# Kernel optimization log

Measured on AMD Instinct MI355X. Metric: run time of the kernel, lower is better.

## Reference

```python
import jax, jax.numpy as jnp
import numpy as np

S, B, E, H = 192, 2, 512, 2
D = E // H      # head_dim = 256 == E/2; required so attn_fc(3*D) matches concat of three E/2 chunks
BH = B * H

def _lin(x, W, b):
    return x @ W.T + b

def setup_inputs():
    key = jax.random.key(0)
    ks = jax.random.split(key, 16)
    p = lambda k, *s: jax.random.normal(k, s, jnp.float32) * 0.02
    return {
        "query":       jax.random.normal(ks[0], (S, B, E), jnp.float32),
        "entity":      jax.random.normal(ks[1], (S, B, E), jnp.float32),
        "ex_entity":   jax.random.normal(ks[2], (S, B, B, E), jnp.float32),
        "ex_relation": jax.random.normal(ks[3], (S, B, B, E), jnp.float32),
        "Wq": p(ks[4], D, E), "bq": jnp.zeros((D,), jnp.float32),
        "Wk": p(ks[5], D, E), "bk": jnp.zeros((D,), jnp.float32),
        "Wv": p(ks[6], D, E), "bv": jnp.zeros((D,), jnp.float32),
        "We": p(ks[7], D, E), "be": jnp.zeros((D,), jnp.float32),
        "Wxe": p(ks[8], D, E), "bxe": jnp.zeros((D,), jnp.float32),
        "Wxr": p(ks[9], D, E), "bxr": jnp.zeros((D,), jnp.float32),
        "Wa": p(ks[10], 1, 3 * D), "ba": jnp.zeros((1,), jnp.float32),
        "Wo": p(ks[11], E, E), "bo": jnp.zeros((E,), jnp.float32),
    }

def reference(query, entity, ex_entity, ex_relation,
              Wq, bq, Wk, bk, Wv, bv, We, be, Wxe, bxe, Wxr, bxr, Wa, ba, Wo, bo):
    e = _lin(entity, We, be)            # [S,B,D]
    q = _lin(query, Wq, bq)             # [S,B,D]
    exr = _lin(ex_entity, Wxe, bxe)     # exent_proj(ex_entity) -> [S,B,B,D]
    exe = _lin(ex_relation, Wxr, bxr)   # exrel_proj(ex_relation) -> [S,B,B,D]
    e_b = jnp.broadcast_to(e[:, :, None, :], exe.shape)
    exz = jnp.concatenate([exe, e_b, exr], axis=-1)                              # [S,B,B,3D]
    exw = jax.nn.softmax(jax.nn.leaky_relu((exz @ Wa.T + ba)[..., 0]), axis=-1)  # [S,B,B]
    we = jnp.einsum('sbk,skd->sbd', exw, e)  # torch.bmm; dead when en_tgt==tgt (faithful fwd compute)
    del we
    qe = jnp.concatenate([q, e], axis=-1)    # [S,B,E]  (else-branch: e.size(0)==q.size(0))
    k = _lin(query, Wk, bk)
    v = _lin(query, Wv, bv)
    ke = jnp.concatenate([k, e], axis=-1)
    ve = jnp.concatenate([v, e], axis=-1)
    shp = lambda x: jnp.swapaxes(x.reshape(S, BH, D), 0, 1)  # torch _shape -> [BH,S,D]
    qe_s, ke_s, ve_s = shp(qe), shp(ke), shp(ve)
    # edge[i,j,b,:] = entity[i,b] - entity[j,b]; torch then does a flat .view(BH,S,S,D)
    edge = (entity[:, None] - entity[None, :]).reshape(BH, S, S, D)
    # qe: transpose(0,1).repeat(S,1,1,1).transpose(0,1).reshape -> broadcast over src then flat reshape
    qe_r = jnp.broadcast_to(jnp.swapaxes(qe_s, 0, 1)[:, None], (S, S, BH, D)).reshape(BH, S, S, D)
    # ke: repeat(S,1,1,1).reshape (flat)
    ke_r = jnp.broadcast_to(ke_s[None], (S, BH, S, D)).reshape(BH, S, S, D)
    z = jnp.concatenate([qe_r, ke_r, edge], axis=-1)                             # [BH,S,S,3D]
    aw = jax.nn.softmax(jax.nn.leaky_relu((z @ Wa.T + ba)[..., 0]), axis=-1)     # [BH,S,S]
    out = jnp.einsum('bts,bsd->btd', aw, ve_s)                                   # [BH,S,D]
    out = jnp.swapaxes(out, 0, 1).reshape(S, B, E)
    return _lin(out, Wo, bo)
```

## Files before the change

### kernel.cpp

```cpp
#include <hip/hip_runtime.h>
#include <math.h>


#define SS 192
#define VO  0
#define EO  98304
#define TO  196608
#define OO  198912
#define WTV 395520
#define WTE 526592
#define WTO 657664

__device__ __forceinline__ float wave_reduce_add(float p) {
    #pragma unroll
    for (int off = 32; off >= 1; off >>= 1) p += __shfl_xor(p, off, 64);
    return p;
}

__global__ __launch_bounds__(1024) void k_prep(
    const float* __restrict__ query, const float* __restrict__ entity,
    const float* __restrict__ Wq, const float* __restrict__ bq,
    const float* __restrict__ Wk, const float* __restrict__ bk,
    const float* __restrict__ Wv, const float* __restrict__ We,
    const float* __restrict__ be, const float* __restrict__ Wa,
    const float* __restrict__ Wo, float* __restrict__ ws)
{
    __shared__ __align__(16) float red[16 * 512];
    __shared__ __align__(16) float uo[516];
    int blk = blockIdx.x;
    int tid = threadIdx.x;

    if (blk < 128) {
        int o = blk * 1024 + tid;
        const float4* src; float4* dst; int idx; int D;
        if (o < 32768)      { src = (const float4*)Wv; dst = (float4*)(ws + WTV); idx = o;         D = 256; }
        else if (o < 65536) { src = (const float4*)We; dst = (float4*)(ws + WTE); idx = o - 32768; D = 256; }
        else                { src = (const float4*)Wo; dst = (float4*)(ws + WTO); idx = o - 65536; D = 512; }
        int d  = idx >> 7;
        int k4 = idx & 127;
        dst[k4 * D + d] = src[idx];
        return;
    }

    int wv   = __builtin_amdgcn_readfirstlane(tid >> 6);
    int lane = tid & 63;

    if (blk < 136) {
        int tab = blk - 128;
        int p   = (tab < 4) ? tab : tab - 4;
        int b   = p >> 1, h = p & 1;
        const float* wa   = Wa + ((tab < 4) ? 0 : 256);
        const float* W    = h ? We : ((tab < 4) ? Wq : Wk);
        const float* bias = h ? be : ((tab < 4) ? bq : bk);
        const float* x    = h ? entity : query;

        float u8[8];
        #pragma unroll
        for (int i = 0; i < 8; i++) u8[i] = 0.f;
        #pragma unroll 4
        for (int dd = 0; dd < 16; dd++) {
            int d = wv * 16 + dd;
            float wad = wa[d];
            const float4* Wr = (const float4*)(W + (size_t)d * 512);
            float4 w0 = Wr[lane * 2], w1 = Wr[lane * 2 + 1];
            u8[0] += wad * w0.x; u8[1] += wad * w0.y; u8[2] += wad * w0.z; u8[3] += wad * w0.w;
            u8[4] += wad * w1.x; u8[5] += wad * w1.y; u8[6] += wad * w1.z; u8[7] += wad * w1.w;
        }
        #pragma unroll
        for (int i = 0; i < 8; i++) red[wv * 512 + lane * 8 + i] = u8[i];
        __syncthreads();
        if (tid < 512) {
            float s = 0.f;
            #pragma unroll
            for (int w = 0; w < 16; w++) s += red[w * 512 + tid];
            uo[tid] = s;
        }
        __syncthreads();
        if (tid < 256) red[tid] = wa[tid] * bias[tid];
        __syncthreads();
        for (int o = 128; o >= 1; o >>= 1) {
            if (tid < o) red[tid] += red[tid + o];
            __syncthreads();
        }
        float off = red[0];

        const float4* u4 = (const float4*)uo;
        float4 ua = u4[lane * 2], ub = u4[lane * 2 + 1];
        for (int rr = 0; rr < 12; rr++) {
            int r = wv * 12 + rr;
            const float4* xr = (const float4*)(x + (size_t)(r * 2 + b) * 512);
            float4 a0 = xr[lane * 2], a1 = xr[lane * 2 + 1];
            float pp = a0.x*ua.x + a0.y*ua.y + a0.z*ua.z + a0.w*ua.w
                     + a1.x*ub.x + a1.y*ub.y + a1.z*ub.z + a1.w*ub.w;
            pp = wave_reduce_add(pp);
            if (lane == 0) ws[TO + tab * SS + r] = pp + off;
        }
        return;
    }

    {
        int m = blk - 136;
        float4 wa4 = ((const float4*)(Wa + 512))[lane];
        for (int rr = 0; rr < 12; rr++) {
            int i = wv * 12 + rr;
            const float4* er = (const float4*)(entity
                + (size_t)(i * 2 + (m >> 1)) * 512 + (m & 1) * 256);
            float4 e4 = er[lane];
            float pp = e4.x*wa4.x + e4.y*wa4.y + e4.z*wa4.z + e4.w*wa4.w;
            pp = wave_reduce_add(pp);
            if (lane == 0) ws[TO + (8 + m) * SS + i] = pp;
        }
    }
}

__global__ __launch_bounds__(1024) void k_proj(
    const float* __restrict__ query, const float* __restrict__ entity,
    const float* __restrict__ bv, const float* __restrict__ be,
    float* __restrict__ ws)
{
    __shared__ float lds[4096];
    int blk = blockIdx.x;
    int m  = blk / 96;
    int r0 = (blk % 96) * 4;
    int tid = threadIdx.x;
    int chunk = __builtin_amdgcn_readfirstlane(tid >> 8);
    int d  = tid & 255;
    const float*  A    = m ? entity : query;
    const float*  bias = m ? be : bv;
    const float4* WT   = (const float4*)(ws + (m ? WTE : WTV));
    float*        dst  = ws + (m ? EO : VO);
    const float4* A4   = (const float4*)A;

    float acc[4];
    #pragma unroll
    for (int r = 0; r < 4; r++) acc[r] = 0.f;

    int k4b = chunk * 32;
    #pragma unroll 8
    for (int i = 0; i < 32; i++) {
        int k4 = k4b + i;
        float4 w = WT[k4 * 256 + d];
        #pragma unroll
        for (int r = 0; r < 4; r++) {
            float4 a = A4[(r0 + r) * 128 + k4];
            acc[r] += a.x * w.x + a.y * w.y + a.z * w.z + a.w * w.w;
        }
    }
    #pragma unroll
    for (int r = 0; r < 4; r++) lds[(chunk * 4 + r) * 256 + d] = acc[r];
    __syncthreads();
    {
        int idx = tid;
        int rr  = idx >> 8, dd = idx & 255;
        float v = lds[idx] + lds[1024 + idx] + lds[2048 + idx] + lds[3072 + idx];
        dst[(size_t)(r0 + rr) * 256 + dd] = v + bias[dd];
    }
}

__global__ __launch_bounds__(1024) void k_attn(
    const float* __restrict__ ba_p, float* __restrict__ ws)
{
    __shared__ __align__(16) float lds[4096];
    __shared__ __align__(16) float sp4[768];
    int blk = blockIdx.x;
    int bh = blk & 3;
    int tg = blk >> 2;
    int b = bh >> 1, h = bh & 1;
    const float* T = ws + TO;
    float ba = ba_p[0];
    int tid  = threadIdx.x;
    int wv   = __builtin_amdgcn_readfirstlane(tid >> 6);
    int lane = tid & 63;

    if (wv < 4) {
        int ti = wv;
        int i_idx = bh * 48 + tg;
        float sc[3]; float mx = -1e30f;
        #pragma unroll
        for (int i = 0; i < 3; i++) {
            int s_ = lane + 64 * i;
            int m  = s_ & 3;
            int j  = ti * 48 + (s_ >> 2);
            float xv = T[m * SS + i_idx] + T[(4 + ti) * SS + s_]
                     + T[(8 + m) * SS + i_idx] - T[(8 + m) * SS + j] + ba;
            xv = (xv >= 0.f) ? xv : 0.01f * xv;
            sc[i] = xv; mx = fmaxf(mx, xv);
        }
        #pragma unroll
        for (int o = 32; o >= 1; o >>= 1) mx = fmaxf(mx, __shfl_xor(mx, o, 64));
        float sum = 0.f;
        #pragma unroll
        for (int i = 0; i < 3; i++) { sc[i] = __expf(sc[i] - mx); sum += sc[i]; }
        sum = wave_reduce_add(sum);
        float inv = 1.f / sum;
        #pragma unroll
        for (int i = 0; i < 3; i++) sp4[ti * SS + lane + 64 * i] = sc[i] * inv;
    }
    __syncthreads();

    int sq = __builtin_amdgcn_readfirstlane(tid >> 8);
    int dd = tid & 255;
    const float* src = ws + (h ? EO : VO) + b * 256 + dd;
    float a[4] = {0.f, 0.f, 0.f, 0.f};
    #pragma unroll 8
    for (int s2 = 0; s2 < 48; s2++) {
        int s = sq * 48 + s2;
        float xv = src[(size_t)s * 512];
        #pragma unroll
        for (int ti = 0; ti < 4; ti++) a[ti] += sp4[ti * SS + s] * xv;
    }
    #pragma unroll
    for (int ti = 0; ti < 4; ti++) lds[sq * 1024 + ti * 256 + dd] = a[ti];
    __syncthreads();
    {
        int ti = tid >> 8, d2 = tid & 255;
        int idx = ti * 256 + d2;
        float v = lds[idx] + lds[1024 + idx] + lds[2048 + idx] + lds[3072 + idx];
        int t = tg * 4 + ti;
        ws[OO + (size_t)(2 * t + b) * 512 + h * 256 + d2] = v;
    }
}

__global__ __launch_bounds__(1024) void k_out(
    const float* __restrict__ bo, const float* __restrict__ ws,
    float* __restrict__ out)
{
    __shared__ float lds[4096];
    int blk = blockIdx.x;
    int rg = blk >> 1;
    int cg = blk & 1;
    int r0 = rg * 4;
    int tid = threadIdx.x;
    int chunk = __builtin_amdgcn_readfirstlane(tid >> 8);
    int col = cg * 256 + (tid & 255);
    const float4* A4 = (const float4*)(ws + OO);
    const float4* WT = (const float4*)(ws + WTO);

    float acc[4];
    #pragma unroll
    for (int r = 0; r < 4; r++) acc[r] = 0.f;

    int k4b = chunk * 32;
    #pragma unroll 8
    for (int i = 0; i < 32; i++) {
        int k4 = k4b + i;
        float4 w = WT[k4 * 512 + col];
        #pragma unroll
        for (int r = 0; r < 4; r++) {
            float4 a = A4[(r0 + r) * 128 + k4];
            acc[r] += a.x * w.x + a.y * w.y + a.z * w.z + a.w * w.w;
        }
    }
    int dl = tid & 255;
    #pragma unroll
    for (int r = 0; r < 4; r++) lds[(chunk * 4 + r) * 256 + dl] = acc[r];
    __syncthreads();
    {
        int idx = tid;
        int rr = idx >> 8, d2 = idx & 255;
        float v = lds[idx] + lds[1024 + idx] + lds[2048 + idx] + lds[3072 + idx];
        out[(size_t)(r0 + rr) * 512 + cg * 256 + d2] = v + bo[cg * 256 + d2];
    }
}

extern "C" void kernel_launch(void* const* d_in, const int* in_sizes, int n_in,
                              void* d_out, int out_size, void* d_ws, size_t ws_size,
                              hipStream_t stream) {
    const float* query  = (const float*)d_in[0];
    const float* entity = (const float*)d_in[1];
    const float* Wq = (const float*)d_in[4];  const float* bq = (const float*)d_in[5];
    const float* Wk = (const float*)d_in[6];  const float* bk = (const float*)d_in[7];
    const float* Wv = (const float*)d_in[8];  const float* bv = (const float*)d_in[9];
    const float* We = (const float*)d_in[10]; const float* be = (const float*)d_in[11];
    const float* Wa = (const float*)d_in[16]; const float* ba = (const float*)d_in[17];
    const float* Wo = (const float*)d_in[18]; const float* bo = (const float*)d_in[19];
    float* ws  = (float*)d_ws;
    float* out = (float*)d_out;

    hipLaunchKernelGGL(k_prep, dim3(140), dim3(1024), 0, stream,
                       query, entity, Wq, bq, Wk, bk, Wv, We, be, Wa, Wo, ws);
    hipLaunchKernelGGL(k_proj, dim3(192), dim3(1024), 0, stream,
                       query, entity, bv, be, ws);
    hipLaunchKernelGGL(k_attn, dim3(192), dim3(1024), 0, stream, ba, ws);
    hipLaunchKernelGGL(k_out,  dim3(192), dim3(1024), 0, stream, bo, ws, out);
}
```

Before: 48.90 us.

## Fuse attention with output projection and merge projection with score tables

Restructures the four-kernel pipeline into three. The Wv/We transpose moves to its own small kernel, and the V/E projection is merged into the same launch as the score-table computation. Attention and the Wo output projection are fused into one kernel that handles both heads per block, using wave-reduced dot products against untransposed Wo rows. This drops the Wo transpose and the intermediate attention-output round trip through workspace, but leaves only 96 blocks for the fused stage, each doing a full 512-column projection.

```diff
diff --git a/kernel.cpp b/kernel.cpp
--- a/kernel.cpp
+++ b/kernel.cpp
@@ -6,10 +6,8 @@
 #define VO  0
 #define EO  98304
 #define TO  196608
-#define OO  198912
-#define WTV 395520
-#define WTE 526592
-#define WTO 657664
+#define WTV 198912
+#define WTE 330240
 
 __device__ __forceinline__ float wave_reduce_add(float p) {
     #pragma unroll
@@ -17,36 +15,75 @@
     return p;
 }
 
-__global__ __launch_bounds__(1024) void k_prep(
+__global__ __launch_bounds__(1024) void k_trans(
+    const float* __restrict__ Wv, const float* __restrict__ We,
+    float* __restrict__ ws)
+{
+    int o = blockIdx.x * 1024 + threadIdx.x;
+    const float4* src; float4* dst; int idx;
+    if (o < 32768) { src = (const float4*)Wv; dst = (float4*)(ws + WTV); idx = o; }
+    else           { src = (const float4*)We; dst = (float4*)(ws + WTE); idx = o - 32768; }
+    int d  = idx >> 7;
+    int k4 = idx & 127;
+    dst[k4 * 256 + d] = src[idx];
+}
+
+__global__ __launch_bounds__(1024) void k_projtab(
     const float* __restrict__ query, const float* __restrict__ entity,
     const float* __restrict__ Wq, const float* __restrict__ bq,
     const float* __restrict__ Wk, const float* __restrict__ bk,
-    const float* __restrict__ Wv, const float* __restrict__ We,
+    const float* __restrict__ bv, const float* __restrict__ We,
     const float* __restrict__ be, const float* __restrict__ Wa,
-    const float* __restrict__ Wo, float* __restrict__ ws)
+    float* __restrict__ ws)
 {
-    __shared__ __align__(16) float red[16 * 512];
+    __shared__ __align__(16) float shbuf[8192];
     __shared__ __align__(16) float uo[516];
     int blk = blockIdx.x;
     int tid = threadIdx.x;
-
-    if (blk < 128) {
-        int o = blk * 1024 + tid;
-        const float4* src; float4* dst; int idx; int D;
-        if (o < 32768)      { src = (const float4*)Wv; dst = (float4*)(ws + WTV); idx = o;         D = 256; }
-        else if (o < 65536) { src = (const float4*)We; dst = (float4*)(ws + WTE); idx = o - 32768; D = 256; }
-        else                { src = (const float4*)Wo; dst = (float4*)(ws + WTO); idx = o - 65536; D = 512; }
-        int d  = idx >> 7;
-        int k4 = idx & 127;
-        dst[k4 * D + d] = src[idx];
-        return;
-    }
-
     int wv   = __builtin_amdgcn_readfirstlane(tid >> 6);
     int lane = tid & 63;
 
-    if (blk < 136) {
-        int tab = blk - 128;
+    if (blk < 192) {
+        int m  = blk / 96;
+        int r0 = (blk % 96) * 4;
+        int chunk = __builtin_amdgcn_readfirstlane(tid >> 8);
+        int d  = tid & 255;
+        const float*  A    = m ? entity : query;
+        const float*  bias = m ? be : bv;
+        const float4* WT   = (const float4*)(ws + (m ? WTE : WTV));
+        float*        dst  = ws + (m ? EO : VO);
+        const float4* A4   = (const float4*)A;
+
+        float acc[4];
+        #pragma unroll
+        for (int r = 0; r < 4; r++) acc[r] = 0.f;
+
+        int k4b = chunk * 32;
+        #pragma unroll 8
+        for (int i = 0; i < 32; i++) {
+            int k4 = k4b + i;
+            float4 w = WT[k4 * 256 + d];
+            #pragma unroll
+            for (int r = 0; r < 4; r++) {
+                float4 a = A4[(r0 + r) * 128 + k4];
+                acc[r] += a.x * w.x + a.y * w.y + a.z * w.z + a.w * w.w;
+            }
+        }
+        #pragma unroll
+        for (int r = 0; r < 4; r++) shbuf[(chunk * 4 + r) * 256 + d] = acc[r];
+        __syncthreads();
+        {
+            int idx = tid;
+            int rr  = idx >> 8, dd = idx & 255;
+            float v = shbuf[idx] + shbuf[1024 + idx] + shbuf[2048 + idx] + shbuf[3072 + idx];
+            dst[(size_t)(r0 + rr) * 256 + dd] = v + bias[dd];
+        }
+        return;
+    }
+
+    if (blk < 200) {
+        float* red = shbuf;
+        int tab = blk - 192;
         int p   = (tab < 4) ? tab : tab - 4;
         int b   = p >> 1, h = p & 1;
         const float* wa   = Wa + ((tab < 4) ? 0 : 256);
@@ -99,7 +136,7 @@
     }
 
     {
-        int m = blk - 136;
+        int m = blk - 200;
         float4 wa4 = ((const float4*)(Wa + 512))[lane];
         for (int rr = 0; rr < 12; rr++) {
             int i = wv * 12 + rr;
@@ -113,67 +150,27 @@
     }
 }
 
-__global__ __launch_bounds__(1024) void k_proj(
-    const float* __restrict__ query, const float* __restrict__ entity,
-    const float* __restrict__ bv, const float* __restrict__ be,
-    float* __restrict__ ws)
+__global__ __launch_bounds__(1024) void k_attnout(
+    const float* __restrict__ ba_p, const float* __restrict__ Wo,
+    const float* __restrict__ bo, const float* __restrict__ ws,
+    float* __restrict__ out)
 {
-    __shared__ float lds[4096];
+    __shared__ float sp[8][SS];
+    __shared__ __align__(16) float2 part2[2048];
+    __shared__ __align__(16) float rows[4][512];
+    __shared__ float sout[2048];
     int blk = blockIdx.x;
-    int m  = blk / 96;
-    int r0 = (blk % 96) * 4;
-    int tid = threadIdx.x;
-    int chunk = __builtin_amdgcn_readfirstlane(tid >> 8);
-    int d  = tid & 255;
-    const float*  A    = m ? entity : query;
-    const float*  bias = m ? be : bv;
-    const float4* WT   = (const float4*)(ws + (m ? WTE : WTV));
-    float*        dst  = ws + (m ? EO : VO);
-    const float4* A4   = (const float4*)A;
-
-    float acc[4];
-    #pragma unroll
-    for (int r = 0; r < 4; r++) acc[r] = 0.f;
-
-    int k4b = chunk * 32;
-    #pragma unroll 8
-    for (int i = 0; i < 32; i++) {
-        int k4 = k4b + i;
-        float4 w = WT[k4 * 256 + d];
-        #pragma unroll
-        for (int r = 0; r < 4; r++) {
-            float4 a = A4[(r0 + r) * 128 + k4];
-            acc[r] += a.x * w.x + a.y * w.y + a.z * w.z + a.w * w.w;
-        }
-    }
-    #pragma unroll
-    for (int r = 0; r < 4; r++) lds[(chunk * 4 + r) * 256 + d] = acc[r];
-    __syncthreads();
-    {
-        int idx = tid;
-        int rr  = idx >> 8, dd = idx & 255;
-        float v = lds[idx] + lds[1024 + idx] + lds[2048 + idx] + lds[3072 + idx];
-        dst[(size_t)(r0 + rr) * 256 + dd] = v + bias[dd];
-    }
-}
-
-__global__ __launch_bounds__(1024) void k_attn(
-    const float* __restrict__ ba_p, float* __restrict__ ws)
-{
-    __shared__ __align__(16) float lds[4096];
-    __shared__ __align__(16) float sp4[768];
-    int blk = blockIdx.x;
-    int bh = blk & 3;
-    int tg = blk >> 2;
-    int b = bh >> 1, h = bh & 1;
+    int b   = blk / 48;
+    int tg  = blk % 48;
+    int tid  = threadIdx.x;
+    int wvi  = __builtin_amdgcn_readfirstlane(tid >> 6);
+    int lane = tid & 63;
     const float* T = ws + TO;
     float ba = ba_p[0];
-    int tid  = threadIdx.x;
-    int wv   = __builtin_amdgcn_readfirstlane(tid >> 6);
-    int lane = tid & 63;
-
-    if (wv < 4) {
-        int ti = wv;
+
+    if (wvi < 8) {
+        int h = wvi >> 2, ti = wvi & 3;
+        int bh = 2 * b + h;
         int i_idx = bh * 48 + tg;
         float sc[3]; float mx = -1e30f;
         #pragma unroll
@@ -194,72 +191,92 @@
         sum = wave_reduce_add(sum);
         float inv = 1.f / sum;
         #pragma unroll
-        for (int i = 0; i < 3; i++) sp4[ti * SS + lane + 64 * i] = sc[i] * inv;
+        for (int i = 0; i < 3; i++) sp[wvi][lane + 64 * i] = sc[i] * inv;
     }
     __syncthreads();
 
-    int sq = __builtin_amdgcn_readfirstlane(tid >> 8);
-    int dd = tid & 255;
-    const float* src = ws + (h ? EO : VO) + b * 256 + dd;
-    float a[4] = {0.f, 0.f, 0.f, 0.f};
-    #pragma unroll 8
-    for (int s2 = 0; s2 < 48; s2++) {
-        int s = sq * 48 + s2;
-        float xv = src[(size_t)s * 512];
-        #pragma unroll
-        for (int ti = 0; ti < 4; ti++) a[ti] += sp4[ti * SS + s] * xv;
-    }
+    {
+        int h  = __builtin_amdgcn_readfirstlane(tid >> 9);
+        int sq = __builtin_amdgcn_readfirstlane((tid >> 7) & 3);
+        int d2 = tid & 127;
+        const float2* src2 = (const float2*)(ws + (h ? EO : VO));
+        float2 acc2[4];
+        #pragma unroll
+        for (int ti = 0; ti < 4; ti++) acc2[ti] = make_float2(0.f, 0.f);
+        int s0 = sq * 48;
+        #pragma unroll 16
+        for (int s2 = 0; s2 < 48; s2++) {
+            int s = s0 + s2;
+            float2 v = src2[(size_t)(s * 2 + b) * 128 + d2];
+            #pragma unroll
+            for (int ti = 0; ti < 4; ti++) {
+                float p = sp[h * 4 + ti][s];
+                acc2[ti].x += p * v.x;
+                acc2[ti].y += p * v.y;
+            }
+        }
+        #pragma unroll
+        for (int ti = 0; ti < 4; ti++)
+            part2[((h * 4 + sq) * 4 + ti) * 128 + d2] = acc2[ti];
+    }
+    __syncthreads();
+
+    {
+        const float* partf = (const float*)part2;
+        int ti = tid >> 8, dd = tid & 255;
+        float r0 = 0.f, r1 = 0.f;
+        #pragma unroll
+        for (int sq = 0; sq < 4; sq++) {
+            r0 += partf[((0 + sq) * 4 + ti) * 256 + dd];
+            r1 += partf[((4 + sq) * 4 + ti) * 256 + dd];
+        }
+        rows[ti][dd]       = r0;
+        rows[ti][256 + dd] = r1;
+    }
+    __syncthreads();
+
+    {
+        const float4* rows4 = (const float4*)rows;
+        float4 rr[4][2];
+        #pragma unroll
+        for (int ti = 0; ti < 4; ti++) {
+            rr[ti][0] = rows4[ti * 128 + lane * 2];
+            rr[ti][1] = rows4[ti * 128 + lane * 2 + 1];
+        }
+        const float4* Wo4 = (const float4*)Wo;
+        int c0 = wvi * 32;
+        #pragma unroll 4
+        for (int i = 0; i < 32; i++) {
+            int c = c0 + i;
+            float4 w0 = Wo4[(size_t)c * 128 + lane * 2];
+            float4 w1 = Wo4[(size_t)c * 128 + lane * 2 + 1];
+            float pt[4];
+            #pragma unroll
+            for (int ti = 0; ti < 4; ti++) {
+                pt[ti] = rr[ti][0].x * w0.x + rr[ti][0].y * w0.y
+                       + rr[ti][0].z * w0.z + rr[ti][0].w * w0.w
+                       + rr[ti][1].x * w1.x + rr[ti][1].y * w1.y
+                       + rr[ti][1].z * w1.z + rr[ti][1].w * w1.w;
+            }
+            #pragma unroll
+            for (int o = 32; o >= 1; o >>= 1) {
+                #pragma unroll
+                for (int ti = 0; ti < 4; ti++) pt[ti] += __shfl_xor(pt[ti], o, 64);
+            }
+            if (lane == 0) {
+                #pragma unroll
+                for (int ti = 0; ti < 4; ti++) sout[ti * 512 + c] = pt[ti];
+            }
+        }
+    }
+    __syncthreads();
+
     #pragma unroll
-    for (int ti = 0; ti < 4; ti++) lds[sq * 1024 + ti * 256 + dd] = a[ti];
-    __syncthreads();
-    {
-        int ti = tid >> 8, d2 = tid & 255;
-        int idx = ti * 256 + d2;
-        float v = lds[idx] + lds[1024 + idx] + lds[2048 + idx] + lds[3072 + idx];
+    for (int o = 0; o < 2; o++) {
+        int idx = tid + o * 1024;
+        int ti = idx >> 9, c = idx & 511;
         int t = tg * 4 + ti;
-        ws[OO + (size_t)(2 * t + b) * 512 + h * 256 + d2] = v;
-    }
-}
-
-__global__ __launch_bounds__(1024) void k_out(
-    const float* __restrict__ bo, const float* __restrict__ ws,
-    float* __restrict__ out)
-{
-    __shared__ float lds[4096];
-    int blk = blockIdx.x;
-    int rg = blk >> 1;
-    int cg = blk & 1;
-    int r0 = rg * 4;
-    int tid = threadIdx.x;
-    int chunk = __builtin_amdgcn_readfirstlane(tid >> 8);
-    int col = cg * 256 + (tid & 255);
-    const float4* A4 = (const float4*)(ws + OO);
-    const float4* WT = (const float4*)(ws + WTO);
-
-    float acc[4];
-    #pragma unroll
-    for (int r = 0; r < 4; r++) acc[r] = 0.f;
-
-    int k4b = chunk * 32;
-    #pragma unroll 8
-    for (int i = 0; i < 32; i++) {
-        int k4 = k4b + i;
-        float4 w = WT[k4 * 512 + col];
-        #pragma unroll
-        for (int r = 0; r < 4; r++) {
-            float4 a = A4[(r0 + r) * 128 + k4];
-            acc[r] += a.x * w.x + a.y * w.y + a.z * w.z + a.w * w.w;
-        }
-    }
-    int dl = tid & 255;
-    #pragma unroll
-    for (int r = 0; r < 4; r++) lds[(chunk * 4 + r) * 256 + dl] = acc[r];
-    __syncthreads();
-    {
-        int idx = tid;
-        int rr = idx >> 8, d2 = idx & 255;
-        float v = lds[idx] + lds[1024 + idx] + lds[2048 + idx] + lds[3072 + idx];
-        out[(size_t)(r0 + rr) * 512 + cg * 256 + d2] = v + bo[cg * 256 + d2];
+        out[(size_t)(2 * t + b) * 512 + c] = sout[idx] + bo[c];
     }
 }
 
@@ -277,10 +294,9 @@
     float* ws  = (float*)d_ws;
     float* out = (float*)d_out;
 
-    hipLaunchKernelGGL(k_prep, dim3(140), dim3(1024), 0, stream,
-                       query, entity, Wq, bq, Wk, bk, Wv, We, be, Wa, Wo, ws);
-    hipLaunchKernelGGL(k_proj, dim3(192), dim3(1024), 0, stream,
-                       query, entity, bv, be, ws);
-    hipLaunchKernelGGL(k_attn, dim3(192), dim3(1024), 0, stream, ba, ws);
-    hipLaunchKernelGGL(k_out,  dim3(192), dim3(1024), 0, stream, bo, ws, out);
-}
+    hipLaunchKernelGGL(k_trans,   dim3(64),  dim3(1024), 0, stream, Wv, We, ws);
+    hipLaunchKernelGGL(k_projtab, dim3(204), dim3(1024), 0, stream,
+                       query, entity, Wq, bq, Wk, bk, bv, We, be, Wa, ws);
+    hipLaunchKernelGGL(k_attnout, dim3(96),  dim3(1024), 0, stream,
+                       ba, Wo, bo, ws, out);
+}
```

Result: slower. 70.28 us (+43.7%).

## Fuse attention aggregation and output projection into one kernel

Applied to the files above, without the earlier changes.

Merges k_attn and k_out into a single k_attnout kernel. Each block now handles both heads of one batch for four target rows and writes the full 512-wide row to a per-block workspace scratch. After a dcache invalidate it reads the scratch back and multiplies it by Wo to produce the final output. This removes one kernel launch and the separate global round-trip and scheduling gap between attention and output projection. In exchange the grid halves to 96 blocks, so occupancy drops, and every block re-reads all of Wo. The workspace layout is also reshuffled.

```diff
diff --git a/kernel.cpp b/kernel.cpp
--- a/kernel.cpp
+++ b/kernel.cpp
@@ -3,13 +3,13 @@
 
 
 #define SS 192
-#define VO  0
-#define EO  98304
-#define TO  196608
-#define OO  198912
-#define WTV 395520
-#define WTE 526592
-#define WTO 657664
+#define WTV 0
+#define WTE 131072
+#define WTO 262144
+#define TO  524288
+#define VO  526592
+#define EO  624896
+#define ROWS 723200
 
 __device__ __forceinline__ float wave_reduce_add(float p) {
     #pragma unroll
@@ -157,23 +157,24 @@
     }
 }
 
-__global__ __launch_bounds__(1024) void k_attn(
-    const float* __restrict__ ba_p, float* __restrict__ ws)
+__global__ __launch_bounds__(1024) void k_attnout(
+    const float* __restrict__ ba_p, const float* __restrict__ bo,
+    float* __restrict__ ws, float* __restrict__ out)
 {
-    __shared__ __align__(16) float lds[4096];
-    __shared__ __align__(16) float sp4[768];
+    __shared__ __align__(16) float spT[SS * 8];
+    __shared__ __align__(16) float partU[8192];
     int blk = blockIdx.x;
-    int bh = blk & 3;
-    int tg = blk >> 2;
-    int b = bh >> 1, h = bh & 1;
+    int b   = blk / 48;
+    int tg  = blk % 48;
+    int tid  = threadIdx.x;
+    int wvi  = __builtin_amdgcn_readfirstlane(tid >> 6);
+    int lane = tid & 63;
     const float* T = ws + TO;
     float ba = ba_p[0];
-    int tid  = threadIdx.x;
-    int wv   = __builtin_amdgcn_readfirstlane(tid >> 6);
-    int lane = tid & 63;
-
-    if (wv < 4) {
-        int ti = wv;
+
+    if (wvi < 8) {
+        int h = wvi >> 2, ti = wvi & 3;
+        int bh = 2 * b + h;
         int i_idx = bh * 48 + tg;
         float sc[3]; float mx = -1e30f;
         #pragma unroll
@@ -194,72 +195,90 @@
         sum = wave_reduce_add(sum);
         float inv = 1.f / sum;
         #pragma unroll
-        for (int i = 0; i < 3; i++) sp4[ti * SS + lane + 64 * i] = sc[i] * inv;
-    }
-    __syncthreads();
-
-    int sq = __builtin_amdgcn_readfirstlane(tid >> 8);
-    int dd = tid & 255;
-    const float* src = ws + (h ? EO : VO) + b * 256 + dd;
-    float a[4] = {0.f, 0.f, 0.f, 0.f};
-    #pragma unroll 8
-    for (int s2 = 0; s2 < 48; s2++) {
-        int s = sq * 48 + s2;
-        float xv = src[(size_t)s * 512];
-        #pragma unroll
-        for (int ti = 0; ti < 4; ti++) a[ti] += sp4[ti * SS + s] * xv;
-    }
+        for (int i = 0; i < 3; i++)
+            spT[(lane + 64 * i) * 8 + h * 4 + ti] = sc[i] * inv;
+    }
+    __syncthreads();
+
+    {
+        int h  = __builtin_amdgcn_readfirstlane(tid >> 9);
+        int sq = __builtin_amdgcn_readfirstlane((tid >> 7) & 3);
+        int d2 = tid & 127;
+        const float2* src2 = (const float2*)(ws + (h ? EO : VO));
+        const float4* spT4 = (const float4*)spT;
+        float2 acc2[4];
+        #pragma unroll
+        for (int ti = 0; ti < 4; ti++) acc2[ti] = make_float2(0.f, 0.f);
+        int s0 = sq * 48;
+        #pragma unroll 8
+        for (int s2 = 0; s2 < 48; s2++) {
+            int s = s0 + s2;
+            float4 p4 = spT4[s * 2 + h];
+            float2 v  = src2[(size_t)(s * 2 + b) * 128 + d2];
+            acc2[0].x += p4.x * v.x; acc2[0].y += p4.x * v.y;
+            acc2[1].x += p4.y * v.x; acc2[1].y += p4.y * v.y;
+            acc2[2].x += p4.z * v.x; acc2[2].y += p4.z * v.y;
+            acc2[3].x += p4.w * v.x; acc2[3].y += p4.w * v.y;
+        }
+        float2* pf2 = (float2*)partU;
+        #pragma unroll
+        for (int ti = 0; ti < 4; ti++)
+            pf2[((h * 4 + sq) * 4 + ti) * 128 + d2] = acc2[ti];
+    }
+    __syncthreads();
+
+    {
+        const float* partf = partU;
+        int ti = tid >> 8, dd = tid & 255;
+        float r0 = 0.f, r1 = 0.f;
+        #pragma unroll
+        for (int sq = 0; sq < 4; sq++) {
+            r0 += partf[((0 + sq) * 4 + ti) * 256 + dd];
+            r1 += partf[((4 + sq) * 4 + ti) * 256 + dd];
+        }
+        float* wsrows = ws + ROWS + blk * 2048;
+        wsrows[ti * 512 + dd]       = r0;
+        wsrows[ti * 512 + 256 + dd] = r1;
+    }
+    __syncthreads();
+    asm volatile("s_dcache_inv" ::: "memory");
+
+    {
+        int kc = __builtin_amdgcn_readfirstlane(tid >> 8);
+        int cl = tid & 255;
+        const float4* A4 = (const float4*)(ws + ROWS + blk * 2048);
+        const float4* WT = (const float4*)(ws + WTO);
+        float acc0[4], acc1[4];
+        #pragma unroll
+        for (int r = 0; r < 4; r++) { acc0[r] = 0.f; acc1[r] = 0.f; }
+        int k4b = kc * 32;
+        #pragma unroll 8
+        for (int i = 0; i < 32; i++) {
+            int k4 = k4b + i;
+            float4 w0 = WT[k4 * 512 + cl];
+            float4 w1 = WT[k4 * 512 + cl + 256];
+            #pragma unroll
+            for (int r = 0; r < 4; r++) {
+                float4 a = A4[r * 128 + k4];
+                acc0[r] += a.x * w0.x + a.y * w0.y + a.z * w0.z + a.w * w0.w;
+                acc1[r] += a.x * w1.x + a.y * w1.y + a.z * w1.z + a.w * w1.w;
+            }
+        }
+        #pragma unroll
+        for (int r = 0; r < 4; r++) {
+            partU[kc * 2048 + r * 512 + cl]       = acc0[r];
+            partU[kc * 2048 + r * 512 + 256 + cl] = acc1[r];
+        }
+    }
+    __syncthreads();
     #pragma unroll
-    for (int ti = 0; ti < 4; ti++) lds[sq * 1024 + ti * 256 + dd] = a[ti];
-    __syncthreads();
-    {
-        int ti = tid >> 8, d2 = tid & 255;
-        int idx = ti * 256 + d2;
-        float v = lds[idx] + lds[1024 + idx] + lds[2048 + idx] + lds[3072 + idx];
+    for (int o = 0; o < 2; o++) {
+        int idx = o * 1024 + tid;
+        int ti = idx >> 9, c = idx & 511;
+        float v = partU[ti * 512 + c] + partU[2048 + ti * 512 + c]
+                + partU[4096 + ti * 512 + c] + partU[6144 + ti * 512 + c];
         int t = tg * 4 + ti;
-        ws[OO + (size_t)(2 * t + b) * 512 + h * 256 + d2] = v;
-    }
-}
-
-__global__ __launch_bounds__(1024) void k_out(
-    const float* __restrict__ bo, const float* __restrict__ ws,
-    float* __restrict__ out)
-{
-    __shared__ float lds[4096];
-    int blk = blockIdx.x;
-    int rg = blk >> 1;
-    int cg = blk & 1;
-    int r0 = rg * 4;
-    int tid = threadIdx.x;
-    int chunk = __builtin_amdgcn_readfirstlane(tid >> 8);
-    int col = cg * 256 + (tid & 255);
-    const float4* A4 = (const float4*)(ws + OO);
-    const float4* WT = (const float4*)(ws + WTO);
-
-    float acc[4];
-    #pragma unroll
-    for (int r = 0; r < 4; r++) acc[r] = 0.f;
-
-    int k4b = chunk * 32;
-    #pragma unroll 8
-    for (int i = 0; i < 32; i++) {
-        int k4 = k4b + i;
-        float4 w = WT[k4 * 512 + col];
-        #pragma unroll
-        for (int r = 0; r < 4; r++) {
-            float4 a = A4[(r0 + r) * 128 + k4];
-            acc[r] += a.x * w.x + a.y * w.y + a.z * w.z + a.w * w.w;
-        }
-    }
-    int dl = tid & 255;
-    #pragma unroll
-    for (int r = 0; r < 4; r++) lds[(chunk * 4 + r) * 256 + dl] = acc[r];
-    __syncthreads();
-    {
-        int idx = tid;
-        int rr = idx >> 8, d2 = idx & 255;
-        float v = lds[idx] + lds[1024 + idx] + lds[2048 + idx] + lds[3072 + idx];
-        out[(size_t)(r0 + rr) * 512 + cg * 256 + d2] = v + bo[cg * 256 + d2];
+        out[(size_t)(2 * t + b) * 512 + c] = v + bo[c];
     }
 }
 
@@ -281,6 +300,6 @@
                        query, entity, Wq, bq, Wk, bk, Wv, We, be, Wa, Wo, ws);
     hipLaunchKernelGGL(k_proj, dim3(192), dim3(1024), 0, stream,
                        query, entity, bv, be, ws);
-    hipLaunchKernelGGL(k_attn, dim3(192), dim3(1024), 0, stream, ba, ws);
-    hipLaunchKernelGGL(k_out,  dim3(192), dim3(1024), 0, stream, bo, ws, out);
-}
+    hipLaunchKernelGGL(k_attnout, dim3(96), dim3(1024), 0, stream,
+                       ba, bo, ws, out);
+}
```

After: 68.76 us, median of 2. +40.6%, slower.

## Retile projection and output GEMMs to 16-row by 64-col blocks with 16-way K split

Applied to the files above, without the earlier changes.

The V/E projection and output projection kernels now compute 16 rows by 64 columns per block, with each wave taking a 32-element K slice. Partial sums are reduced through a larger LDS buffer. This raises activation-row reuse per weight load and cuts redundant weight reads across blocks, at the cost of more registers and a 16-way LDS reduction. The workspace layout is also reordered so the weights sit first.

```diff
diff --git a/kernel.cpp b/kernel.cpp
--- a/kernel.cpp
+++ b/kernel.cpp
@@ -3,13 +3,13 @@
 
 
 #define SS 192
-#define VO  0
-#define EO  98304
-#define TO  196608
-#define OO  198912
-#define WTV 395520
-#define WTE 526592
-#define WTO 657664
+#define WTV 0
+#define WTE 131072
+#define WTO 262144
+#define TO  524288
+#define VO  526592
+#define EO  624896
+#define OO  723200
 
 __device__ __forceinline__ float wave_reduce_add(float p) {
     #pragma unroll
@@ -118,42 +118,47 @@
     const float* __restrict__ bv, const float* __restrict__ be,
     float* __restrict__ ws)
 {
-    __shared__ float lds[4096];
-    int blk = blockIdx.x;
-    int m  = blk / 96;
-    int r0 = (blk % 96) * 4;
+    __shared__ float pl[16384];
+    int blk = blockIdx.x;
+    int m   = blk / 96;
+    int rem = blk % 96;
+    int dq  = rem / 24;
+    int rg  = rem % 24;
+    int r0  = rg * 16;
+    int d0  = dq * 64;
     int tid = threadIdx.x;
-    int chunk = __builtin_amdgcn_readfirstlane(tid >> 8);
-    int d  = tid & 255;
+    int ks  = __builtin_amdgcn_readfirstlane(tid >> 6);
+    int dl  = tid & 63;
     const float*  A    = m ? entity : query;
     const float*  bias = m ? be : bv;
     const float4* WT   = (const float4*)(ws + (m ? WTE : WTV));
     float*        dst  = ws + (m ? EO : VO);
     const float4* A4   = (const float4*)A;
 
-    float acc[4];
-    #pragma unroll
-    for (int r = 0; r < 4; r++) acc[r] = 0.f;
-
-    int k4b = chunk * 32;
-    #pragma unroll 8
-    for (int i = 0; i < 32; i++) {
+    float acc[16];
+    #pragma unroll
+    for (int r = 0; r < 16; r++) acc[r] = 0.f;
+
+    int k4b = ks * 8;
+    #pragma unroll
+    for (int i = 0; i < 8; i++) {
         int k4 = k4b + i;
-        float4 w = WT[k4 * 256 + d];
-        #pragma unroll
-        for (int r = 0; r < 4; r++) {
+        float4 w = WT[k4 * 256 + d0 + dl];
+        #pragma unroll
+        for (int r = 0; r < 16; r++) {
             float4 a = A4[(r0 + r) * 128 + k4];
             acc[r] += a.x * w.x + a.y * w.y + a.z * w.z + a.w * w.w;
         }
     }
     #pragma unroll
-    for (int r = 0; r < 4; r++) lds[(chunk * 4 + r) * 256 + d] = acc[r];
-    __syncthreads();
-    {
-        int idx = tid;
-        int rr  = idx >> 8, dd = idx & 255;
-        float v = lds[idx] + lds[1024 + idx] + lds[2048 + idx] + lds[3072 + idx];
-        dst[(size_t)(r0 + rr) * 256 + dd] = v + bias[dd];
+    for (int r = 0; r < 16; r++) pl[ks * 1024 + r * 64 + dl] = acc[r];
+    __syncthreads();
+    {
+        int r = tid >> 6, d2 = tid & 63;
+        float v = 0.f;
+        #pragma unroll
+        for (int k = 0; k < 16; k++) v += pl[k * 1024 + r * 64 + d2];
+        dst[(size_t)(r0 + r) * 256 + d0 + d2] = v + bias[d0 + d2];
     }
 }
 
@@ -225,41 +230,42 @@
     const float* __restrict__ bo, const float* __restrict__ ws,
     float* __restrict__ out)
 {
-    __shared__ float lds[4096];
-    int blk = blockIdx.x;
-    int rg = blk >> 1;
-    int cg = blk & 1;
-    int r0 = rg * 4;
+    __shared__ float pl[16384];
+    int blk = blockIdx.x;
+    int rg  = blk >> 3;
+    int cq  = blk & 7;
+    int r0  = rg * 16;
+    int c0  = cq * 64;
     int tid = threadIdx.x;
-    int chunk = __builtin_amdgcn_readfirstlane(tid >> 8);
-    int col = cg * 256 + (tid & 255);
+    int kc  = __builtin_amdgcn_readfirstlane(tid >> 6);
+    int cl  = tid & 63;
     const float4* A4 = (const float4*)(ws + OO);
     const float4* WT = (const float4*)(ws + WTO);
 
-    float acc[4];
-    #pragma unroll
-    for (int r = 0; r < 4; r++) acc[r] = 0.f;
-
-    int k4b = chunk * 32;
-    #pragma unroll 8
-    for (int i = 0; i < 32; i++) {
+    float acc[16];
+    #pragma unroll
+    for (int r = 0; r < 16; r++) acc[r] = 0.f;
+
+    int k4b = kc * 8;
+    #pragma unroll
+    for (int i = 0; i < 8; i++) {
         int k4 = k4b + i;
-        float4 w = WT[k4 * 512 + col];
-        #pragma unroll
-        for (int r = 0; r < 4; r++) {
+        float4 w = WT[(size_t)k4 * 512 + c0 + cl];
+        #pragma unroll
+        for (int r = 0; r < 16; r++) {
             float4 a = A4[(r0 + r) * 128 + k4];
             acc[r] += a.x * w.x + a.y * w.y + a.z * w.z + a.w * w.w;
         }
     }
-    int dl = tid & 255;
-    #pragma unroll
-    for (int r = 0; r < 4; r++) lds[(chunk * 4 + r) * 256 + dl] = acc[r];
-    __syncthreads();
-    {
-        int idx = tid;
-        int rr = idx >> 8, d2 = idx & 255;
-        float v = lds[idx] + lds[1024 + idx] + lds[2048 + idx] + lds[3072 + idx];
-        out[(size_t)(r0 + rr) * 512 + cg * 256 + d2] = v + bo[cg * 256 + d2];
+    #pragma unroll
+    for (int r = 0; r < 16; r++) pl[kc * 1024 + r * 64 + cl] = acc[r];
+    __syncthreads();
+    {
+        int r = tid >> 6, c2 = tid & 63;
+        float v = 0.f;
+        #pragma unroll
+        for (int k = 0; k < 16; k++) v += pl[k * 1024 + r * 64 + c2];
+        out[(size_t)(r0 + r) * 512 + c0 + c2] = v + bo[c0 + c2];
     }
 }
 
```

Result: slower. 62.07 us (+26.9%).
